# Kernel tuning notes

Measured on AMD Instinct MI355X. Metric: run time of the kernel, lower is better.

Reference implementation:

```python
import jax, jax.numpy as jnp
import numpy as np

D_MODEL, HIDDEN, H, NB = 1024, 128, 16, 32
B, L = 4, 4096


def setup_inputs() -> dict:
    key = jax.random.key(0)
    ks = jax.random.split(key, 6)
    theta_path = jax.random.normal(ks[0], (B, L, H, NB), dtype=jnp.float32)
    content_emb = jax.random.normal(ks[1], (B, L, D_MODEL), dtype=jnp.float32)
    # params (log_Pi init 0.0; final linear weight scaled by 0.01, bias 0, as in torch init)
    log_Pi = jnp.zeros((H, NB), dtype=jnp.float32)
    W1 = jax.random.normal(ks[2], (D_MODEL, HIDDEN), dtype=jnp.float32) / np.sqrt(D_MODEL)
    b1 = jnp.zeros((HIDDEN,), dtype=jnp.float32)
    W2 = (jax.random.normal(ks[3], (HIDDEN, H * NB), dtype=jnp.float32) / np.sqrt(HIDDEN)) * 0.01
    b2 = jnp.zeros((H * NB,), dtype=jnp.float32)
    return {"theta_path": theta_path, "content_emb": content_emb,
            "log_Pi": log_Pi, "W1": W1, "b1": b1, "W2": W2, "b2": b2}


def _affine_combine(c1, c2):
    a1, u1 = c1
    a2, u2 = c2
    return a2 * a1, a2 * u1 + u2


def reference(theta_path, content_emb, log_Pi, W1, b1, W2, b2):
    Bx, Lx, Hx, NBx = theta_path.shape
    # log_R_head: Linear -> GELU(exact) -> Linear, then clamp
    h = jax.nn.gelu(content_emb @ W1 + b1, approximate=False)
    log_R = jnp.clip((h @ W2 + b2).reshape(Bx, Lx, Hx, NBx), -5.0, 5.0)
    R = jnp.exp(log_R)
    # wrapped innovation nu = atan2(sin(-theta), cos(-theta))
    nu = jnp.arctan2(jnp.sin(-theta_path), jnp.cos(-theta_path))
    Pi = jnp.exp(log_Pi)[None, None]            # [1,1,H,NB]
    K = Pi / jnp.maximum(Pi + R, 1e-8)
    alpha = 1.0 - K
    u = K * nu
    # affine recurrence d_t = alpha_t * d_{t-1} + u_t, parallel scan over L
    _, d = jax.lax.associative_scan(_affine_combine, (alpha, u), axis=1)
    return theta_path + d, jnp.broadcast_to(Pi, R.shape), K, R
```

## Files before the change

### kernel.cpp

```cpp
#include <hip/hip_runtime.h>
#include <math.h>

#define B_   4
#define L_   4096
#define C_   512
#define DM_  1024
#define HID_ 128
#define M_   (B_*L_)
#define NC_  256
#define CT_  16

typedef __attribute__((ext_vector_type(8))) short short8;
typedef __attribute__((ext_vector_type(4))) float f32x4;

__device__ __forceinline__ unsigned short f2bf(float f) {
  unsigned u = __float_as_uint(f);
  u += 0x7fffu + ((u >> 16) & 1u);
  return (unsigned short)(u >> 16);
}

__device__ __forceinline__ float wrap_neg(float th) {
  return 6.283185307179586f * rintf(th * 0.15915494309189535f) - th;
}

__global__ __launch_bounds__(256) void k_prep(const float* __restrict__ W1,
                                              const float* __restrict__ W2,
                                              unsigned short* __restrict__ W1T,
                                              unsigned short* __restrict__ W2T) {
  int idx = blockIdx.x * 256 + threadIdx.x;
  if (idx < DM_ * HID_) {
    int n = idx >> 10, k = idx & 1023;
    W1T[idx] = f2bf(W1[(size_t)k * HID_ + n]);
  }
  int i2 = idx - DM_ * HID_;
  if (i2 >= 0 && i2 < HID_ * C_) {
    int n = i2 >> 7, k = i2 & 127;
    W2T[i2] = f2bf(W2[(size_t)k * C_ + n]);
  }
}

__global__ __launch_bounds__(512) void k_mega(const float* __restrict__ X,
                                              const unsigned short* __restrict__ W1T,
                                              const float* __restrict__ b1,
                                              const unsigned short* __restrict__ W2T,
                                              const float* __restrict__ b2,
                                              const float* __restrict__ logPi,
                                              const float* __restrict__ theta,
                                              float* __restrict__ out1,
                                              float* __restrict__ out2,
                                              float* __restrict__ out3,
                                              float* __restrict__ Ab,
                                              float* __restrict__ Ub) {
  __shared__ char lds[16896];
  const int tid  = threadIdx.x;
  const int m0   = blockIdx.x * 32;
  const int lane = tid & 63;
  const int wave = tid >> 6;
  const int wr   = wave >> 2;
  const int wc   = wave & 3;
  const int fr   = lane & 15;
  const int kg   = lane >> 4;

  const int srow = tid >> 4;
  const int sk4  = tid & 15;
  const float* xsrc = X + (size_t)(m0 + srow) * DM_ + sk4 * 4;
  char* swr = lds + srow * 128 + ((sk4 << 3) ^ ((srow & 7) << 4));

  const unsigned short* w1p0 = W1T + (size_t)(wc * 32 + fr) * DM_ + kg * 8;
  const unsigned short* w1p1 = W1T + (size_t)(wc * 32 + 16 + fr) * DM_ + kg * 8;

  f32x4 acc0 = {0.f, 0.f, 0.f, 0.f};
  f32x4 acc1 = {0.f, 0.f, 0.f, 0.f};

  {
    f32x4 xv = __builtin_nontemporal_load((const f32x4*)xsrc);
    unsigned p0 = f2bf(xv[0]) | ((unsigned)f2bf(xv[1]) << 16);
    unsigned p1 = f2bf(xv[2]) | ((unsigned)f2bf(xv[3]) << 16);
    uint2 pk = {p0, p1};
    *(uint2*)swr = pk;
  }
  __syncthreads();

  short8 bc[4], bn[4];
  bc[0] = *(const short8*)(w1p0);
  bc[1] = *(const short8*)(w1p1);
  bc[2] = *(const short8*)(w1p0 + 32);
  bc[3] = *(const short8*)(w1p1 + 32);

  const int arow = wr * 16 + fr;
  char* ard = lds + arow * 128;

  for (int it = 0; it < 16; ++it) {
    const int cur = it & 1;
    f32x4 xv;
    if (it < 15) {
      xv = __builtin_nontemporal_load((const f32x4*)(xsrc + (it + 1) * 64));
      const unsigned short* p0 = w1p0 + (it + 1) * 64;
      const unsigned short* p1 = w1p1 + (it + 1) * 64;
      bn[0] = *(const short8*)(p0);
      bn[1] = *(const short8*)(p1);
      bn[2] = *(const short8*)(p0 + 32);
      bn[3] = *(const short8*)(p1 + 32);
    }
#pragma unroll
    for (int ks = 0; ks < 2; ++ks) {
      short8 a = *(const short8*)(ard + cur * 4096 +
                                  (((ks * 4 + kg) << 4) ^ ((arow & 7) << 4)));
      acc0 = __builtin_amdgcn_mfma_f32_16x16x32_bf16(a, bc[ks * 2 + 0], acc0, 0, 0, 0);
      acc1 = __builtin_amdgcn_mfma_f32_16x16x32_bf16(a, bc[ks * 2 + 1], acc1, 0, 0, 0);
    }
    if (it < 15) {
      unsigned p0 = f2bf(xv[0]) | ((unsigned)f2bf(xv[1]) << 16);
      unsigned p1 = f2bf(xv[2]) | ((unsigned)f2bf(xv[3]) << 16);
      uint2 pk = {p0, p1};
      *(uint2*)(swr + (1 - cur) * 4096) = pk;
      __syncthreads();
#pragma unroll
      for (int q = 0; q < 4; ++q) bc[q] = bn[q];
    }
  }

#pragma unroll
  for (int j = 0; j < 2; ++j) {
    int col = wc * 32 + j * 16 + fr;
    float bb = b1[col];
    f32x4 av = (j == 0) ? acc0 : acc1;
#pragma unroll
    for (int r = 0; r < 4; ++r) {
      int row = wr * 16 + kg * 4 + r;
      float x = av[r] + bb;
      float g = 0.5f * x * (1.0f + erff(x * 0.70710678f));
      *(unsigned short*)(lds + 8192 + row * 272 + col * 2) = f2bf(g);
    }
  }
  __syncthreads();

  const int bidx = blockIdx.x >> 7;
  const int ch   = ((m0 & 4095) >> 4) + wr;
  const size_t chbase = ((size_t)(bidx * NC_ + ch)) * C_;
  const int colbase = wc * 16 + fr;
  const unsigned short* w2p = W2T + (size_t)colbase * HID_ + kg * 8;
  const char* hrd = lds + 8192 + (wr * 16 + fr) * 272;
  const size_t throw0 = (size_t)(m0 + wr * 16 + kg * 4) * C_;

  short8 c2[4], n2[4];
#pragma unroll
  for (int ks = 0; ks < 4; ++ks) c2[ks] = *(const short8*)(w2p + ks * 32);
  float thc[4], thn[4];
#pragma unroll
  for (int r = 0; r < 4; ++r) thc[r] = theta[throw0 + (size_t)r * C_ + colbase];

  for (int nc = 0; nc < 8; ++nc) {
    const int col = nc * 64 + colbase;
    if (nc < 7) {
#pragma unroll
      for (int ks = 0; ks < 4; ++ks)
        n2[ks] = *(const short8*)(w2p + (size_t)(nc + 1) * 64 * HID_ + ks * 32);
#pragma unroll
      for (int r = 0; r < 4; ++r)
        thn[r] = theta[throw0 + (size_t)r * C_ + col + 64];
    }
    float Pi = expf(logPi[col]);
    float bb = b2[col];

    f32x4 a2 = {0.f, 0.f, 0.f, 0.f};
#pragma unroll
    for (int ks = 0; ks < 4; ++ks) {
      short8 a = *(const short8*)(hrd + ks * 64 + kg * 16);
      a2 = __builtin_amdgcn_mfma_f32_16x16x32_bf16(a, c2[ks], a2, 0, 0, 0);
    }

    float A = 1.f, U = 0.f;
#pragma unroll
    for (int r = 0; r < 4; ++r) {
      int row = m0 + wr * 16 + kg * 4 + r;
      float lr = a2[r] + bb;
      lr = fminf(5.0f, fmaxf(-5.0f, lr));
      float R = expf(lr);
      float K = Pi / fmaxf(Pi + R, 1e-8f);
      size_t o = (size_t)row * C_ + col;
      __builtin_nontemporal_store(Pi, &out1[o]);
      out2[o] = K;
      __builtin_nontemporal_store(R, &out3[o]);
      float nu = wrap_neg(thc[r]);
      float a = 1.f - K;
      U = a * U + K * nu;
      A = a * A;
    }
    float oA = __shfl_xor(A, 16), oU = __shfl_xor(U, 16);
    if ((kg & 1) == 0) { U = oA * U + oU; A = oA * A; }
    else               { U = A * oU + U;  A = A * oA; }
    oA = __shfl_xor(A, 32); oU = __shfl_xor(U, 32);
    if ((kg & 2) == 0) { U = oA * U + oU; A = oA * A; }
    else               { U = A * oU + U;  A = A * oA; }
    if (kg == 0) { Ab[chbase + col] = A; Ub[chbase + col] = U; }

    if (nc < 7) {
#pragma unroll
      for (int ks = 0; ks < 4; ++ks) c2[ks] = n2[ks];
#pragma unroll
      for (int r = 0; r < 4; ++r) thc[r] = thn[r];
    }
  }
}

__global__ __launch_bounds__(256) void k_scan2(const float* __restrict__ Ab,
                                               const float* __restrict__ Ub,
                                               float* __restrict__ D0) {
  __shared__ float cA[16][17], cU[16][17], carry[16][17];
  const int tid = threadIdx.x;
  const int b   = blockIdx.x >> 5;
  const int c0  = (blockIdx.x & 31) * 16;
  const int c_l = tid & 15, s = tid >> 4;
  const int c   = c0 + c_l;
  float A = 1.f, U = 0.f;
#pragma unroll
  for (int k = 0; k < 16; ++k) {
    size_t o = ((size_t)(b * NC_ + s * 16 + k)) * C_ + c;
    float a = Ab[o], u = Ub[o];
    U = a * U + u; A *= a;
  }
  cA[s][c_l] = A; cU[s][c_l] = U;
  __syncthreads();
  if (tid < 16) {
    float P = 0.f;
#pragma unroll
    for (int ss = 0; ss < 16; ++ss) {
      carry[ss][tid] = P;
      P = cA[ss][tid] * P + cU[ss][tid];
    }
  }
  __syncthreads();
  float d = carry[s][c_l];
#pragma unroll
  for (int k = 0; k < 16; ++k) {
    size_t o = ((size_t)(b * NC_ + s * 16 + k)) * C_ + c;
    D0[o] = d;
    d = Ab[o] * d + Ub[o];
  }
}

__global__ __launch_bounds__(256) void k_scan3(const float* __restrict__ Kv,
                                               const float* __restrict__ theta,
                                               const float* __restrict__ D0,
                                               float* __restrict__ out0) {
  const int b  = blockIdx.x / NC_;
  const int ch = blockIdx.x % NC_;
  const int c  = blockIdx.y * 256 + threadIdx.x;
  size_t base = ((size_t)b * L_ + (size_t)ch * CT_) * C_ + c;
  float d = D0[((size_t)(b * NC_ + ch)) * C_ + c];
#pragma unroll 4
  for (int j = 0; j < CT_; ++j) {
    size_t idx = base + (size_t)j * C_;
    float k  = Kv[idx];
    float th = theta[idx];
    float nu = wrap_neg(th);
    d = (1.f - k) * d + k * nu;
    __builtin_nontemporal_store(th + d, &out0[idx]);
  }
}

extern "C" void kernel_launch(void* const* d_in, const int* in_sizes, int n_in,
                              void* d_out, int out_size, void* d_ws, size_t ws_size,
                              hipStream_t stream) {
  const float* theta = (const float*)d_in[0];
  const float* X     = (const float*)d_in[1];
  const float* logPi = (const float*)d_in[2];
  const float* W1    = (const float*)d_in[3];
  const float* b1    = (const float*)d_in[4];
  const float* W2    = (const float*)d_in[5];
  const float* b2    = (const float*)d_in[6];

  float* out = (float*)d_out;
  const size_t S = (size_t)M_ * C_;
  float* out0 = out;
  float* out1 = out + S;
  float* out2 = out + 2 * S;
  float* out3 = out + 3 * S;

  unsigned short* W1T = (unsigned short*)d_ws;
  unsigned short* W2T = W1T + (size_t)DM_ * HID_;
  float* Ab = (float*)(W2T + (size_t)HID_ * C_);
  float* Ub = Ab + (size_t)B_ * NC_ * C_;
  float* D0 = Ub + (size_t)B_ * NC_ * C_;

  hipLaunchKernelGGL(k_prep, dim3(768), dim3(256), 0, stream, W1, W2, W1T, W2T);
  hipLaunchKernelGGL(k_mega, dim3(M_ / 32), dim3(512), 0, stream,
                     X, W1T, b1, W2T, b2, logPi, theta, out1, out2, out3, Ab, Ub);
  hipLaunchKernelGGL(k_scan2, dim3(B_ * 32), dim3(256), 0, stream, Ab, Ub, D0);
  hipLaunchKernelGGL(k_scan3, dim3(B_ * NC_, 2), dim3(256), 0, stream, out2, theta, D0, out0);
}
```

Baseline: 89.23 us.

## Halve mega-kernel tile, preload X and theta into registers, vectorize scan3

The mega kernel now processes 16 rows per 256-thread block instead of 32 rows per 512 threads. It loads its entire X slice and all theta values into registers up front, so global latency is exposed once rather than per iteration and occupancy granularity improves. The final scan kernel switches to float4 loads and stores with 4 channels per thread. The trade-off is heavy register pressure (64 X floats plus 32 theta floats per thread), which may cut occupancy, and W1 tiles are now fetched twice as often per output row.

Measured after the change: 99.55 us. 11.6% more time.

```diff
diff --git a/kernel.cpp b/kernel.cpp
--- a/kernel.cpp
+++ b/kernel.cpp
@@ -39,7 +39,7 @@
   }
 }
 
-__global__ __launch_bounds__(512) void k_mega(const float* __restrict__ X,
+__global__ __launch_bounds__(256) void k_mega(const float* __restrict__ X,
                                               const unsigned short* __restrict__ W1T,
                                               const float* __restrict__ b1,
                                               const unsigned short* __restrict__ W2T,
@@ -51,21 +51,32 @@
                                               float* __restrict__ out3,
                                               float* __restrict__ Ab,
                                               float* __restrict__ Ub) {
-  __shared__ char lds[16896];
+  __shared__ char lds[8448];
   const int tid  = threadIdx.x;
-  const int m0   = blockIdx.x * 32;
+  const int m0   = blockIdx.x * 16;
   const int lane = tid & 63;
-  const int wave = tid >> 6;
-  const int wr   = wave >> 2;
-  const int wc   = wave & 3;
+  const int wc   = tid >> 6;
   const int fr   = lane & 15;
   const int kg   = lane >> 4;
 
   const int srow = tid >> 4;
   const int sk4  = tid & 15;
   const float* xsrc = X + (size_t)(m0 + srow) * DM_ + sk4 * 4;
+  f32x4 xr[16];
+#pragma unroll
+  for (int it = 0; it < 16; ++it)
+    xr[it] = __builtin_nontemporal_load((const f32x4*)(xsrc + it * 64));
+
+  const int colbase = wc * 16 + fr;
+  const size_t throw0 = (size_t)(m0 + kg * 4) * C_;
+  float thr[8][4];
+#pragma unroll
+  for (int nc = 0; nc < 8; ++nc)
+#pragma unroll
+    for (int r = 0; r < 4; ++r)
+      thr[nc][r] = theta[throw0 + (size_t)r * C_ + nc * 64 + colbase];
+
   char* swr = lds + srow * 128 + ((sk4 << 3) ^ ((srow & 7) << 4));
-
   const unsigned short* w1p0 = W1T + (size_t)(wc * 32 + fr) * DM_ + kg * 8;
   const unsigned short* w1p1 = W1T + (size_t)(wc * 32 + 16 + fr) * DM_ + kg * 8;
 
@@ -73,47 +84,42 @@
   f32x4 acc1 = {0.f, 0.f, 0.f, 0.f};
 
   {
-    f32x4 xv = __builtin_nontemporal_load((const f32x4*)xsrc);
-    unsigned p0 = f2bf(xv[0]) | ((unsigned)f2bf(xv[1]) << 16);
-    unsigned p1 = f2bf(xv[2]) | ((unsigned)f2bf(xv[3]) << 16);
-    uint2 pk = {p0, p1};
+    uint2 pk = { f2bf(xr[0][0]) | ((unsigned)f2bf(xr[0][1]) << 16),
+                 f2bf(xr[0][2]) | ((unsigned)f2bf(xr[0][3]) << 16) };
     *(uint2*)swr = pk;
   }
-  __syncthreads();
-
   short8 bc[4], bn[4];
   bc[0] = *(const short8*)(w1p0);
   bc[1] = *(const short8*)(w1p1);
   bc[2] = *(const short8*)(w1p0 + 32);
   bc[3] = *(const short8*)(w1p1 + 32);
-
-  const int arow = wr * 16 + fr;
+  __syncthreads();
+
+  const int arow = fr;
   char* ard = lds + arow * 128;
 
+#pragma unroll
   for (int it = 0; it < 16; ++it) {
     const int cur = it & 1;
-    f32x4 xv;
     if (it < 15) {
-      xv = __builtin_nontemporal_load((const f32x4*)(xsrc + (it + 1) * 64));
       const unsigned short* p0 = w1p0 + (it + 1) * 64;
       const unsigned short* p1 = w1p1 + (it + 1) * 64;
       bn[0] = *(const short8*)(p0);
       bn[1] = *(const short8*)(p1);
       bn[2] = *(const short8*)(p0 + 32);
       bn[3] = *(const short8*)(p1 + 32);
+      uint2 pk = { f2bf(xr[it + 1][0]) | ((unsigned)f2bf(xr[it + 1][1]) << 16),
+                   f2bf(xr[it + 1][2]) | ((unsigned)f2bf(xr[it + 1][3]) << 16) };
+      *(uint2*)(swr + (1 - cur) * 2048) = pk;
     }
 #pragma unroll
     for (int ks = 0; ks < 2; ++ks) {
-      short8 a = *(const short8*)(ard + cur * 4096 +
+      short8 a = *(const short8*)(ard + cur * 2048 +
                                   (((ks * 4 + kg) << 4) ^ ((arow & 7) << 4)));
       acc0 = __builtin_amdgcn_mfma_f32_16x16x32_bf16(a, bc[ks * 2 + 0], acc0, 0, 0, 0);
       acc1 = __builtin_amdgcn_mfma_f32_16x16x32_bf16(a, bc[ks * 2 + 1], acc1, 0, 0, 0);
     }
     if (it < 15) {
-      unsigned p0 = f2bf(xv[0]) | ((unsigned)f2bf(xv[1]) << 16);
-      unsigned p1 = f2bf(xv[2]) | ((unsigned)f2bf(xv[3]) << 16);
-      uint2 pk = {p0, p1};
-      *(uint2*)(swr + (1 - cur) * 4096) = pk;
       __syncthreads();
 #pragma unroll
       for (int q = 0; q < 4; ++q) bc[q] = bn[q];
@@ -127,38 +133,31 @@
     f32x4 av = (j == 0) ? acc0 : acc1;
 #pragma unroll
     for (int r = 0; r < 4; ++r) {
-      int row = wr * 16 + kg * 4 + r;
+      int row = kg * 4 + r;
       float x = av[r] + bb;
       float g = 0.5f * x * (1.0f + erff(x * 0.70710678f));
-      *(unsigned short*)(lds + 8192 + row * 272 + col * 2) = f2bf(g);
-    }
-  }
-  __syncthreads();
-
-  const int bidx = blockIdx.x >> 7;
-  const int ch   = ((m0 & 4095) >> 4) + wr;
+      *(unsigned short*)(lds + 4096 + row * 272 + col * 2) = f2bf(g);
+    }
+  }
+  __syncthreads();
+
+  const int bidx = blockIdx.x >> 8;
+  const int ch   = blockIdx.x & 255;
   const size_t chbase = ((size_t)(bidx * NC_ + ch)) * C_;
-  const int colbase = wc * 16 + fr;
   const unsigned short* w2p = W2T + (size_t)colbase * HID_ + kg * 8;
-  const char* hrd = lds + 8192 + (wr * 16 + fr) * 272;
-  const size_t throw0 = (size_t)(m0 + wr * 16 + kg * 4) * C_;
+  const char* hrd = lds + 4096 + fr * 272;
 
   short8 c2[4], n2[4];
 #pragma unroll
   for (int ks = 0; ks < 4; ++ks) c2[ks] = *(const short8*)(w2p + ks * 32);
-  float thc[4], thn[4];
-#pragma unroll
-  for (int r = 0; r < 4; ++r) thc[r] = theta[throw0 + (size_t)r * C_ + colbase];
-
+
+#pragma unroll
   for (int nc = 0; nc < 8; ++nc) {
     const int col = nc * 64 + colbase;
     if (nc < 7) {
 #pragma unroll
       for (int ks = 0; ks < 4; ++ks)
         n2[ks] = *(const short8*)(w2p + (size_t)(nc + 1) * 64 * HID_ + ks * 32);
-#pragma unroll
-      for (int r = 0; r < 4; ++r)
-        thn[r] = theta[throw0 + (size_t)r * C_ + col + 64];
     }
     float Pi = expf(logPi[col]);
     float bb = b2[col];
@@ -173,7 +172,7 @@
     float A = 1.f, U = 0.f;
 #pragma unroll
     for (int r = 0; r < 4; ++r) {
-      int row = m0 + wr * 16 + kg * 4 + r;
+      int row = m0 + kg * 4 + r;
       float lr = a2[r] + bb;
       lr = fminf(5.0f, fmaxf(-5.0f, lr));
       float R = expf(lr);
@@ -182,7 +181,7 @@
       __builtin_nontemporal_store(Pi, &out1[o]);
       out2[o] = K;
       __builtin_nontemporal_store(R, &out3[o]);
-      float nu = wrap_neg(thc[r]);
+      float nu = wrap_neg(thr[nc][r]);
       float a = 1.f - K;
       U = a * U + K * nu;
       A = a * A;
@@ -198,8 +197,6 @@
     if (nc < 7) {
 #pragma unroll
       for (int ks = 0; ks < 4; ++ks) c2[ks] = n2[ks];
-#pragma unroll
-      for (int r = 0; r < 4; ++r) thc[r] = thn[r];
     }
   }
 }
@@ -244,19 +241,26 @@
                                                const float* __restrict__ theta,
                                                const float* __restrict__ D0,
                                                float* __restrict__ out0) {
-  const int b  = blockIdx.x / NC_;
-  const int ch = blockIdx.x % NC_;
-  const int c  = blockIdx.y * 256 + threadIdx.x;
-  size_t base = ((size_t)b * L_ + (size_t)ch * CT_) * C_ + c;
-  float d = D0[((size_t)(b * NC_ + ch)) * C_ + c];
+  const int g  = blockIdx.x * 256 + threadIdx.x;
+  const int cg = g & 127;
+  const int ch = (g >> 7) & 255;
+  const int b  = g >> 15;
+  const int c0 = cg * 4;
+  size_t base = ((size_t)b * L_ + (size_t)ch * CT_) * C_ + c0;
+  f32x4 d = *(const f32x4*)(D0 + ((size_t)(b * NC_ + ch)) * C_ + c0);
 #pragma unroll 4
   for (int j = 0; j < CT_; ++j) {
     size_t idx = base + (size_t)j * C_;
-    float k  = Kv[idx];
-    float th = theta[idx];
-    float nu = wrap_neg(th);
-    d = (1.f - k) * d + k * nu;
-    __builtin_nontemporal_store(th + d, &out0[idx]);
+    f32x4 k  = *(const f32x4*)(Kv + idx);
+    f32x4 th = *(const f32x4*)(theta + idx);
+    f32x4 o;
+#pragma unroll
+    for (int q = 0; q < 4; ++q) {
+      float nu = wrap_neg(th[q]);
+      d[q] = (1.f - k[q]) * d[q] + k[q] * nu;
+      o[q] = th[q] + d[q];
+    }
+    __builtin_nontemporal_store(o, (f32x4*)(out0 + idx));
   }
 }
 
@@ -285,8 +289,9 @@
   float* D0 = Ub + (size_t)B_ * NC_ * C_;
 
   hipLaunchKernelGGL(k_prep, dim3(768), dim3(256), 0, stream, W1, W2, W1T, W2T);
-  hipLaunchKernelGGL(k_mega, dim3(M_ / 32), dim3(512), 0, stream,
+  hipLaunchKernelGGL(k_mega, dim3(M_ / 16), dim3(256), 0, stream,
                      X, W1T, b1, W2T, b2, logPi, theta, out1, out2, out3, Ab, Ub);
   hipLaunchKernelGGL(k_scan2, dim3(B_ * 32), dim3(256), 0, stream, Ab, Ub, D0);
-  hipLaunchKernelGGL(k_scan3, dim3(B_ * NC_, 2), dim3(256), 0, stream, out2, theta, D0, out0);
-}
+  hipLaunchKernelGGL(k_scan3, dim3(M_ * C_ / 64 / 256), dim3(256), 0, stream,
+                     out2, theta, D0, out0);
+}
```
